# Kernel optimization log

Hardware: AMD Instinct MI355X
Metric: run time of the kernel (lower is better)

Reference implementation:

```python
import jax, jax.numpy as jnp
import numpy as np

N, D, H, E = 50000, 128, 128, 800000


def setup_inputs() -> dict:
    key = jax.random.key(0)
    ks = jax.random.split(key, 12)
    p = lambda k, shape: jax.random.normal(k, shape, dtype=jnp.float32) * 0.02
    z = lambda n: jnp.zeros((n,), jnp.float32)
    return {
        "x1": jax.random.normal(ks[0], (N, D), dtype=jnp.float32),
        "edge_index1": jax.random.randint(ks[1], (2, E), 0, N, dtype=jnp.int32),
        "x2": jax.random.normal(ks[2], (N, D), dtype=jnp.float32),
        "edge_index2": jax.random.randint(ks[3], (2, E), 0, N, dtype=jnp.int32),
        "enc_w1": p(ks[4], (D, H)), "enc_b1": z(H),
        "enc_w2": p(ks[5], (H, H)), "enc_b2": z(H),
        "conv1_w": p(ks[6], (H, H)), "conv1_b": z(H),
        "conv2_w": p(ks[7], (H, H)), "conv2_b": z(H),
        "sim_w1": p(ks[8], (4 * H, H)), "sim_b1": z(H),
        "sim_w2": p(ks[9], (H, 1)), "sim_b2": z(1),
    }


def reference(x1, edge_index1, x2, edge_index2,
              enc_w1, enc_b1, enc_w2, enc_b2,
              conv1_w, conv1_b, conv2_w, conv2_b,
              sim_w1, sim_b1, sim_w2, sim_b2):
    def gcn(x, ei, W, b):
        row, col = ei[0], ei[1]            # [E], [E]
        h = x @ W + b                      # [N, H]
        n = x.shape[0]
        deg = jax.ops.segment_sum(jnp.ones(row.shape[0], h.dtype), row, num_segments=n)
        dis = jnp.where(deg > 0, deg ** -0.5, 0.0)   # deg^-0.5, inf -> 0
        norm = dis[row] * dis[col]         # [E]
        msg = h[col] * norm[:, None]       # gather + per-edge scale, [E, H]
        return jax.ops.segment_sum(msg, row, num_segments=n)  # scatter-add

    def embed(x, ei):
        h = jax.nn.relu(x @ enc_w1 + enc_b1) @ enc_w2 + enc_b2  # encoder MLP
        h = jax.nn.relu(gcn(h, ei, conv1_w, conv1_b))
        h = jax.nn.relu(gcn(h, ei, conv2_w, conv2_b))
        return h.mean(axis=0)              # mean pooling -> [H]

    g1 = embed(x1, edge_index1)
    g2 = embed(x2, edge_index2)
    c = jnp.concatenate([g1, g2, jnp.abs(g1 - g2), g1 * g2], axis=-1)  # [4H]
    return jax.nn.relu(c @ sim_w1 + sim_b1) @ sim_w2 + sim_b2          # [1]
```

## Files before the change

### kernel.cpp

```cpp
#include <hip/hip_runtime.h>

#define HD 128
#define FP8_SCALE 8192.0f
#define FP8_INV   (1.0f / 8192.0f)

typedef _Float16 f16x8 __attribute__((ext_vector_type(8)));
typedef float f32x4 __attribute__((ext_vector_type(4)));
typedef float f32x2 __attribute__((ext_vector_type(2)));

static __device__ __forceinline__ unsigned char f32_to_fp8(float v) {
  return (unsigned char)(__builtin_amdgcn_cvt_pk_fp8_f32(v, v, 0, false) & 0xff);
}

__device__ __forceinline__ void role_map(int bi, int S, int k, int& role, int& rid) {
  int q = bi / k, rem = bi - q * k;
  if (rem == 0 && q < S) { role = 1; rid = q; }
  else { role = 0; int na = q + (rem ? 1 : 0); if (na > S) na = S; rid = bi - na; }
}

__global__ void k_wcvt(const float* __restrict__ w0, const float* __restrict__ w1,
                       const float* __restrict__ w2, const float* __restrict__ w3,
                       _Float16* __restrict__ Wf) {
  int m = blockIdx.x >> 3;
  const float* Wg = (m == 0) ? w0 : (m == 1) ? w1 : (m == 2) ? w2 : w3;
  int idx0 = (blockIdx.x & 7) * 2048 + threadIdx.x * 8;
  float4 u0 = *(const float4*)(Wg + idx0);
  float4 u1 = *(const float4*)(Wg + idx0 + 4);
  int k = idx0 >> 7, n0 = idx0 & 127;
  int kc = k >> 5, q2 = (k >> 3) & 3, j = k & 7;
  _Float16* dst = Wf + (size_t)m * 16384;
  float vv[8] = {u0.x, u0.y, u0.z, u0.w, u1.x, u1.y, u1.z, u1.w};
  #pragma unroll
  for (int d = 0; d < 8; ++d) {
    int n = n0 + d;
    dst[(size_t)(((n >> 4) * 4 + kc) * 64 + 16 * q2 + (n & 15)) * 8 + j] = (_Float16)vv[d];
  }
}

__device__ __forceinline__ void deg_core(int rid, int degB,
    const int* __restrict__ ei0, const int* __restrict__ ei1, int E, int N,
    int* __restrict__ deg2, unsigned short* __restrict__ slot) {
  int g = (rid >= degB);
  int cb = rid - g * degB;
  const int* rows = g ? ei1 : ei0;
  int* deg = deg2 + g * N;
  unsigned short* sl = slot + (size_t)g * E;
  int base = (cb * 256 + threadIdx.x) * 4;
  if (base + 3 < E) {
    int4 r = *(const int4*)(rows + base);
    union { unsigned short us[4]; uint2 v; } s;
    s.us[0] = (unsigned short)atomicAdd(&deg[r.x], 1);
    s.us[1] = (unsigned short)atomicAdd(&deg[r.y], 1);
    s.us[2] = (unsigned short)atomicAdd(&deg[r.z], 1);
    s.us[3] = (unsigned short)atomicAdd(&deg[r.w], 1);
    *(uint2*)(sl + base) = s.v;
  } else {
    for (int e = base; e < E; ++e)
      sl[e] = (unsigned short)atomicAdd(&deg[rows[e]], 1);
  }
}

__device__ __forceinline__ void fill_core(int rid, int fillB,
    const int* __restrict__ ei0, const int* __restrict__ ei1, int E, int N,
    const int* __restrict__ offs, const int* __restrict__ partials,
    const unsigned short* __restrict__ slot, unsigned short* __restrict__ csr_col) {
  int g = (rid >= fillB);
  int cb = rid - g * fillB;
  const int* eg = (g ? ei1 : ei0);
  const int* ob = offs + g * N;
  const unsigned short* sl = slot + (size_t)g * E;
  int gN = g * N;
  int base = (cb * 256 + threadIdx.x) * 4;
  if (base + 3 < E) {
    int4 r = *(const int4*)(eg + base);
    int4 c = *(const int4*)(eg + E + base);
    uint2 sv = *(const uint2*)(sl + base);
    csr_col[ob[r.x] + partials[(gN + r.x) >> 8] + (sv.x & 0xffff)] = (unsigned short)c.x;
    csr_col[ob[r.y] + partials[(gN + r.y) >> 8] + (sv.x >> 16)]    = (unsigned short)c.y;
    csr_col[ob[r.z] + partials[(gN + r.z) >> 8] + (sv.y & 0xffff)] = (unsigned short)c.z;
    csr_col[ob[r.w] + partials[(gN + r.w) >> 8] + (sv.y >> 16)]    = (unsigned short)c.w;
  } else {
    for (int e = base; e < E; ++e)
      csr_col[ob[eg[e]] + partials[(gN + eg[e]) >> 8] + sl[e]] = (unsigned short)eg[E + e];
  }
}

__device__ __forceinline__ void gemm_core(_Float16* lds, int bi,
    const _Float16* __restrict__ Ab, const _Float16* __restrict__ Wf,
    const float* __restrict__ bias, const float* __restrict__ scale,
    unsigned char* __restrict__ Cv, int Ntot) {
  const int tid = threadIdx.x;
  #pragma unroll
  for (int i = 0; i < 8; ++i)
    *(float4*)&lds[tid * 8 + i * 2048] = *(const float4*)&Wf[tid * 8 + i * 2048];
  __syncthreads();

  const int lane = tid & 63, wave = tid >> 6;
  const int n16 = lane & 15, q = lane >> 4;
  const int rowbase = bi * 128 + wave * 32;

  int arow[2];
  #pragma unroll
  for (int t = 0; t < 2; ++t) {
    int r = rowbase + 16 * t + n16;
    arow[t] = (r < Ntot) ? r : (Ntot - 1);
  }
  f32x4 acc[2][8];
  #pragma unroll
  for (int t = 0; t < 2; ++t)
    #pragma unroll
    for (int nt = 0; nt < 8; ++nt) acc[t][nt] = (f32x4){0.f, 0.f, 0.f, 0.f};

  #pragma unroll
  for (int kc = 0; kc < 4; ++kc) {
    f16x8 a[2];
    #pragma unroll
    for (int t = 0; t < 2; ++t)
      a[t] = *(const f16x8*)(Ab + (size_t)arow[t] * HD + kc * 32 + q * 8);
    #pragma unroll
    for (int nt = 0; nt < 8; ++nt) {
      f16x8 b = *(const f16x8*)&lds[(size_t)((nt * 4 + kc) * 64 + lane) * 8];
      #pragma unroll
      for (int t = 0; t < 2; ++t)
        acc[t][nt] = __builtin_amdgcn_mfma_f32_16x16x32_f16(a[t], b, acc[t][nt], 0, 0, 0);
    }
  }
  float bv[8];
  #pragma unroll
  for (int nt = 0; nt < 8; ++nt) bv[nt] = bias[nt * 16 + n16];
  #pragma unroll
  for (int t = 0; t < 2; ++t) {
    #pragma unroll
    for (int r = 0; r < 4; ++r) {
      int row = rowbase + 16 * t + 4 * q + r;
      if (row < Ntot) {
        float s = scale[row];
        #pragma unroll
        for (int nt = 0; nt < 8; ++nt) {
          float v = (acc[t][nt][r] + bv[nt]) * s;
          Cv[(size_t)row * HD + nt * 16 + n16] = f32_to_fp8(v * FP8_SCALE);
        }
      }
    }
  }
}

__device__ __forceinline__ void chain_core(_Float16* act, int bi,
    const float* __restrict__ x0, const float* __restrict__ x1,
    const _Float16* __restrict__ Wf0, const _Float16* __restrict__ Wf1,
    const float* __restrict__ b1, const float* __restrict__ b2,
    _Float16* __restrict__ H, int N, int Ntot) {
  const int tid = threadIdx.x;
  const int lane = tid & 63, wave = tid >> 6;
  const int n16 = lane & 15, q = lane >> 4;
  const int rowbase = bi * 128 + wave * 32;
  _Float16* wact = act + wave * 4352;

  int arow[2];
  #pragma unroll
  for (int t = 0; t < 2; ++t) {
    int r = rowbase + 16 * t + n16;
    arow[t] = (r < Ntot) ? r : (Ntot - 1);
  }
  f32x4 acc[2][8];
  #pragma unroll
  for (int t = 0; t < 2; ++t)
    #pragma unroll
    for (int nt = 0; nt < 8; ++nt) acc[t][nt] = (f32x4){0.f, 0.f, 0.f, 0.f};

  #pragma unroll
  for (int kc = 0; kc < 4; ++kc) {
    f16x8 a[2];
    #pragma unroll
    for (int t = 0; t < 2; ++t) {
      int r = arow[t];
      const float* src = (r < N) ? (x0 + (size_t)r * HD) : (x1 + (size_t)(r - N) * HD);
      float4 u0 = *(const float4*)(src + kc * 32 + q * 8);
      float4 u1 = *(const float4*)(src + kc * 32 + q * 8 + 4);
      union { _Float16 h[8]; f16x8 v; } tmp;
      tmp.h[0] = (_Float16)u0.x; tmp.h[1] = (_Float16)u0.y;
      tmp.h[2] = (_Float16)u0.z; tmp.h[3] = (_Float16)u0.w;
      tmp.h[4] = (_Float16)u1.x; tmp.h[5] = (_Float16)u1.y;
      tmp.h[6] = (_Float16)u1.z; tmp.h[7] = (_Float16)u1.w;
      a[t] = tmp.v;
    }
    #pragma unroll
    for (int nt = 0; nt < 8; ++nt) {
      f16x8 b = *(const f16x8*)&Wf0[(size_t)((nt * 4 + kc) * 64 + lane) * 8];
      #pragma unroll
      for (int t = 0; t < 2; ++t)
        acc[t][nt] = __builtin_amdgcn_mfma_f32_16x16x32_f16(a[t], b, acc[t][nt], 0, 0, 0);
    }
  }
  {
    float bv[8];
    #pragma unroll
    for (int nt = 0; nt < 8; ++nt) bv[nt] = b1[nt * 16 + n16];
    #pragma unroll
    for (int t = 0; t < 2; ++t)
      #pragma unroll
      for (int r = 0; r < 4; ++r)
        #pragma unroll
        for (int nt = 0; nt < 8; ++nt)
          wact[(16 * t + 4 * q + r) * 136 + nt * 16 + n16] =
              (_Float16)fmaxf(acc[t][nt][r] + bv[nt], 0.f);
  }

  #pragma unroll
  for (int t = 0; t < 2; ++t)
    #pragma unroll
    for (int nt = 0; nt < 8; ++nt) acc[t][nt] = (f32x4){0.f, 0.f, 0.f, 0.f};
  #pragma unroll
  for (int kc = 0; kc < 4; ++kc) {
    f16x8 a[2];
    #pragma unroll
    for (int t = 0; t < 2; ++t)
      a[t] = *(const f16x8*)&wact[(16 * t + n16) * 136 + kc * 32 + q * 8];
    #pragma unroll
    for (int nt = 0; nt < 8; ++nt) {
      f16x8 b = *(const f16x8*)&Wf1[(size_t)((nt * 4 + kc) * 64 + lane) * 8];
      #pragma unroll
      for (int t = 0; t < 2; ++t)
        acc[t][nt] = __builtin_amdgcn_mfma_f32_16x16x32_f16(a[t], b, acc[t][nt], 0, 0, 0);
    }
  }
  {
    float bv[8];
    #pragma unroll
    for (int nt = 0; nt < 8; ++nt) bv[nt] = b2[nt * 16 + n16];
    #pragma unroll
    for (int t = 0; t < 2; ++t)
      #pragma unroll
      for (int r = 0; r < 4; ++r) {
        int row = rowbase + 16 * t + 4 * q + r;
        if (row < Ntot)
          #pragma unroll
          for (int nt = 0; nt < 8; ++nt)
            H[(size_t)row * HD + nt * 16 + n16] = (_Float16)(acc[t][nt][r] + bv[nt]);
      }
  }
}

template<bool POOL>
__device__ __forceinline__ void agg_core(float* red, int rid,
    const unsigned char* __restrict__ T8, const int* __restrict__ offs,
    const int* __restrict__ partials, const unsigned short* __restrict__ csr_col,
    const float* __restrict__ dis, _Float16* __restrict__ out,
    float* __restrict__ poolrep, int N, int Ntot, int Etot) {
  const int lane = threadIdx.x & 63;
  const int wave = threadIdx.x >> 6;
  const int gw = rid * 4 + wave;
  const int sub = lane >> 4, c16 = lane & 15;

  float ax[8];
  #pragma unroll
  for (int j = 0; j < 8; ++j) ax[j] = 0.f;

  const int beg = offs[gw] + partials[gw >> 8];
  const int end = (gw + 1 == Ntot) ? Etot : (offs[gw + 1] + partials[(gw + 1) >> 8]);
  const uint2* Tg = (const uint2*)(T8 + (size_t)(gw >= N ? N : 0) * HD);
  for (int e = beg; e < end; e += 16) {
    uint2 v[4];
    #pragma unroll
    for (int gp = 0; gp < 4; ++gp) {
      v[gp] = make_uint2(0, 0);
      if (e + 4 * gp < end) {
        int eg = e + 4 * gp + sub;
        bool valid = (eg < end);
        int ce = valid ? eg : (end - 1);
        int col = csr_col[ce];
        uint2 tv = Tg[(size_t)col * 16 + c16];
        if (valid) v[gp] = tv;
      }
    }
    #pragma unroll
    for (int gp = 0; gp < 4; ++gp) {
      f32x2 p0 = __builtin_amdgcn_cvt_pk_f32_fp8((int)v[gp].x, false);
      f32x2 p1 = __builtin_amdgcn_cvt_pk_f32_fp8((int)v[gp].x, true);
      f32x2 p2 = __builtin_amdgcn_cvt_pk_f32_fp8((int)v[gp].y, false);
      f32x2 p3 = __builtin_amdgcn_cvt_pk_f32_fp8((int)v[gp].y, true);
      ax[0] += p0.x; ax[1] += p0.y;
      ax[2] += p1.x; ax[3] += p1.y;
      ax[4] += p2.x; ax[5] += p2.y;
      ax[6] += p3.x; ax[7] += p3.y;
    }
  }

  #pragma unroll
  for (int j = 0; j < 8; ++j) {
    ax[j] += __shfl_xor(ax[j], 32, 64);
    ax[j] += __shfl_xor(ax[j], 16, 64);
  }
  float dr = dis[gw] * FP8_INV;
  #pragma unroll
  for (int j = 0; j < 8; ++j) ax[j] = fmaxf(ax[j] * dr, 0.f);

  if (!POOL) {
    if (sub == 0) {
      union { uint4 u; _Float16 h[8]; } o;
      #pragma unroll
      for (int j = 0; j < 8; ++j) o.h[j] = (_Float16)ax[j];
      ((uint4*)out)[(size_t)gw * 16 + c16] = o.u;
    }
  } else {
    if (sub == 0) {
      *(float4*)&red[wave * 128 + c16 * 8]     = make_float4(ax[0], ax[1], ax[2], ax[3]);
      *(float4*)&red[wave * 128 + c16 * 8 + 4] = make_float4(ax[4], ax[5], ax[6], ax[7]);
    }
    __syncthreads();
    int t = threadIdx.x;
    if (t < 128) {
      float s = red[t] + red[128 + t] + red[256 + t] + red[384 + t];
      int g = (rid * 4 >= N) ? 1 : 0;
      atomicAdd(&poolrep[(size_t)((rid & 15) * 2 + g) * 128 + t], s);
    }
  }
}

__global__ __launch_bounds__(256, 4) void k_d1(
    const float* __restrict__ x0, const float* __restrict__ x1,
    const _Float16* __restrict__ Wf, const float* __restrict__ b1,
    const float* __restrict__ b2, _Float16* __restrict__ H,
    const int* __restrict__ ei0, const int* __restrict__ ei1, int E, int N, int Ntot,
    int* __restrict__ deg2, unsigned short* __restrict__ slot, int G, int A, int degB) {
  __shared__ _Float16 act[4 * 4352];
  int role, rid;
  role_map(blockIdx.x, G, (A + G) / G, role, rid);
  if (role == 1)
    chain_core(act, rid, x0, x1, Wf, Wf + 16384, b1, b2, H, N, Ntot);
  else
    deg_core(rid, degB, ei0, ei1, E, N, deg2, slot);
}

__global__ __launch_bounds__(256, 2) void k_scan(
    const int* __restrict__ deg2, int* __restrict__ offs, int* __restrict__ partials,
    float* __restrict__ dis, int Ntot, int scanB, int* __restrict__ ctr) {
  __shared__ int s[512];
  __shared__ int lastFlag;
  int rid = blockIdx.x, t = threadIdx.x;
  int i = rid * 256 + t;
  int v = (i < Ntot) ? deg2[i] : 0;
  s[t] = v;
  __syncthreads();
  #pragma unroll
  for (int off = 1; off < 256; off <<= 1) {
    int x = (t >= off) ? s[t - off] : 0;
    __syncthreads();
    s[t] += x;
    __syncthreads();
  }
  if (i < Ntot) {
    offs[i] = s[t] - v;
    dis[i] = (v > 0) ? (1.0f / sqrtf((float)v)) : 0.0f;
  }
  if (t == 255) partials[rid] = s[255];
  __syncthreads();
  if (t == 0) {
    __threadfence();
    lastFlag = (atomicAdd(ctr, 1) == scanB - 1);
  }
  __syncthreads();
  if (lastFlag) {
    __threadfence();
    volatile int* vp = partials;
    int P = scanB;
    int v0 = (t < P) ? vp[t] : 0;
    int v1 = (t + 256 < P) ? vp[t + 256] : 0;
    __syncthreads();
    s[t] = v0;
    s[t + 256] = v1;
    __syncthreads();
    #pragma unroll
    for (int off = 1; off < 256; off <<= 1) {
      int x0 = (t >= off) ? s[t - off] : 0;
      int x1 = (t >= off) ? s[256 + t - off] : 0;
      __syncthreads();
      s[t] += x0;
      s[256 + t] += x1;
      __syncthreads();
    }
    int tot0 = s[255];
    if (t < P) partials[t] = s[t] - v0;
    if (t + 256 < P) partials[t + 256] = s[256 + t] + tot0 - v1;
  }
}

__global__ __launch_bounds__(256, 4) void k_conv1_fill(
    const _Float16* __restrict__ Ain, const _Float16* __restrict__ Wf,
    const float* __restrict__ bias, const float* __restrict__ dis,
    unsigned char* __restrict__ Cout, int Ntot, int G,
    const int* __restrict__ ei0, const int* __restrict__ ei1, int E, int N,
    const int* __restrict__ offs, const int* __restrict__ partials,
    const unsigned short* __restrict__ slot, unsigned short* __restrict__ csr_col,
    int fillB) {
  __shared__ _Float16 lds[16384];
  int role, rid;
  role_map(blockIdx.x, G, 3, role, rid);
  if (role == 1)
    gemm_core(lds, rid, Ain, Wf, bias, dis, Cout, Ntot);
  else
    fill_core(rid, fillB, ei0, ei1, E, N, offs, partials, slot, csr_col);
}

__global__ __launch_bounds__(256) void k_agg(
    const unsigned char* __restrict__ T8, const int* __restrict__ offs,
    const int* __restrict__ partials, const unsigned short* __restrict__ csr_col,
    const float* __restrict__ dis, _Float16* __restrict__ out, int N, int Ntot, int Etot) {
  agg_core<false>(nullptr, blockIdx.x, T8, offs, partials, csr_col, dis,
                  out, nullptr, N, Ntot, Etot);
}

__global__ __launch_bounds__(256, 4) void k_gemm(
    const _Float16* __restrict__ Ain, const _Float16* __restrict__ Wf,
    const float* __restrict__ bias, const float* __restrict__ dis,
    unsigned char* __restrict__ Cout, int Ntot) {
  __shared__ _Float16 lds[16384];
  gemm_core(lds, blockIdx.x, Ain, Wf, bias, dis, Cout, Ntot);
}

__global__ __launch_bounds__(256) void k_agg_pool(
    const unsigned char* __restrict__ T8, const int* __restrict__ offs,
    const int* __restrict__ partials, const unsigned short* __restrict__ csr_col,
    const float* __restrict__ dis, float* __restrict__ poolrep,
    int N, int Ntot, int Etot) {
  __shared__ float red[512];
  agg_core<true>(red, blockIdx.x, T8, offs, partials, csr_col, dis,
                 nullptr, poolrep, N, Ntot, Etot);
}

__global__ void k_final(const float* __restrict__ poolrep,
                        const float* __restrict__ W1, const float* __restrict__ b1,
                        const float* __restrict__ W2, const float* __restrict__ b2,
                        float* __restrict__ out, float invN) {
  __shared__ float cs[512];
  __shared__ float red[2];
  int t = threadIdx.x;
  float g1 = 0.f, g2 = 0.f;
  #pragma unroll
  for (int r = 0; r < 16; ++r) {
    g1 += poolrep[r * 256 + t];
    g2 += poolrep[r * 256 + 128 + t];
  }
  g1 *= invN;
  g2 *= invN;
  cs[t] = g1;
  cs[128 + t] = g2;
  cs[256 + t] = fabsf(g1 - g2);
  cs[384 + t] = g1 * g2;
  __syncthreads();
  float acc = b1[t];
  #pragma unroll 8
  for (int i = 0; i < 512; ++i) acc = fmaf(cs[i], W1[(size_t)i * HD + t], acc);
  float h = fmaxf(acc, 0.f);
  float v = h * W2[t];
  #pragma unroll
  for (int off = 32; off > 0; off >>= 1) v += __shfl_down(v, off, 64);
  if ((t & 63) == 0) red[t >> 6] = v;
  __syncthreads();
  if (t == 0) out[0] = red[0] + red[1] + b2[0];
}

extern "C" void kernel_launch(void* const* d_in, const int* in_sizes, int n_in,
                              void* d_out, int out_size, void* d_ws, size_t ws_size,
                              hipStream_t stream) {
  const float* x1     = (const float*)d_in[0];
  const int*   ei1    = (const int*)d_in[1];
  const float* x2     = (const float*)d_in[2];
  const int*   ei2    = (const int*)d_in[3];
  const float* W_in[4] = {(const float*)d_in[4], (const float*)d_in[6],
                          (const float*)d_in[8], (const float*)d_in[10]};
  const float* B_in[4] = {(const float*)d_in[5], (const float*)d_in[7],
                          (const float*)d_in[9], (const float*)d_in[11]};
  const float* sim_w1 = (const float*)d_in[12];
  const float* sim_b1 = (const float*)d_in[13];
  const float* sim_w2 = (const float*)d_in[14];
  const float* sim_b2 = (const float*)d_in[15];

  const int N = in_sizes[0] / HD;
  const int E = in_sizes[1] / 2;
  const int Ntot = 2 * N;

  _Float16* sp = (_Float16*)d_ws;
  _Float16* bufA = sp; sp += (size_t)Ntot * HD;
  _Float16* bufC = sp; sp += (size_t)Ntot * HD;
  unsigned char* bufT8 = (unsigned char*)sp;
  sp += (size_t)Ntot * HD / 2;
  _Float16* WfB  = sp; sp += 4 * 16384;
  float* fp = (float*)sp;
  float* dis     = fp; fp += Ntot;
  float* poolrep = fp; fp += 16 * 256;
  int* ip = (int*)fp;
  int* ctrs     = ip; ip += 8;
  int* deg2     = ip; ip += Ntot;
  int* offs     = ip; ip += Ntot;
  int* partials = ip; ip += 512;
  ip = (int*)(((uintptr_t)ip + 15) & ~(uintptr_t)15);
  unsigned short* slot = (unsigned short*)ip;
  unsigned short* csr_col = slot + 2 * (size_t)E;

  const int G1    = (Ntot + 127) / 128;
  const int scanB = (Ntot + 255) / 256;
  const int aggB  = Ntot / 4;
  const int degB  = ((E + 3) / 4 + 255) / 256;
  const int fillB = degB;

  hipMemsetAsync(poolrep, 0, (16 * 256 + 8 + Ntot) * sizeof(float), stream);

  k_wcvt<<<32, 256, 0, stream>>>(W_in[0], W_in[1], W_in[2], W_in[3], WfB);

  k_d1<<<2 * degB + G1, 256, 0, stream>>>(
      x1, x2, WfB, B_in[0], B_in[1], bufA, ei1, ei2, E, N, Ntot,
      deg2, slot, G1, 2 * degB, degB);

  k_scan<<<scanB, 256, 0, stream>>>(deg2, offs, partials, dis, Ntot, scanB, ctrs);

  k_conv1_fill<<<2 * fillB + G1, 256, 0, stream>>>(
      bufA, WfB + 2 * 16384, B_in[2], dis, bufT8, Ntot, G1,
      ei1, ei2, E, N, offs, partials, slot, csr_col, fillB);

  k_agg<<<aggB, 256, 0, stream>>>(bufT8, offs, partials, csr_col, dis, bufC, N, Ntot, 2 * E);

  k_gemm<<<G1, 256, 0, stream>>>(bufC, WfB + 3 * 16384, B_in[3], dis, bufT8, Ntot);

  k_agg_pool<<<aggB, 256, 0, stream>>>(bufT8, offs, partials, csr_col, dis, poolrep,
                                       N, Ntot, 2 * E);

  k_final<<<1, 128, 0, stream>>>(poolrep, sim_w1, sim_b1, sim_w2, sim_b2,
                                 (float*)d_out, 1.0f / (float)N);
}
```

Before: 387.5 us.

## Split degree counting into own kernel, fuse scan with encoder chain; widen aggregation unroll

Degree counting becomes a standalone kernel, and the prefix scan is merged with the encoder MLP chain into a single launch via role mapping. This hides the scan behind the GEMM work instead of running it as a separate serial kernel. The aggregation loop also now processes 32 edges per iteration instead of 16, putting more gathers in flight. The cost is higher register use in the aggregation kernel. The scan blocks now reuse the chain's shared memory buffer, and the chain now runs after degree counting rather than overlapping with it.

```diff
diff --git a/kernel.cpp b/kernel.cpp
--- a/kernel.cpp
+++ b/kernel.cpp
@@ -37,9 +37,10 @@
   }
 }
 
-__device__ __forceinline__ void deg_core(int rid, int degB,
+__global__ __launch_bounds__(256) void k_deg(
     const int* __restrict__ ei0, const int* __restrict__ ei1, int E, int N,
-    int* __restrict__ deg2, unsigned short* __restrict__ slot) {
+    int* __restrict__ deg2, unsigned short* __restrict__ slot, int degB) {
+  int rid = blockIdx.x;
   int g = (rid >= degB);
   int cb = rid - g * degB;
   const int* rows = g ? ei1 : ei0;
@@ -241,103 +242,22 @@
   }
 }
 
-template<bool POOL>
-__device__ __forceinline__ void agg_core(float* red, int rid,
-    const unsigned char* __restrict__ T8, const int* __restrict__ offs,
-    const int* __restrict__ partials, const unsigned short* __restrict__ csr_col,
-    const float* __restrict__ dis, _Float16* __restrict__ out,
-    float* __restrict__ poolrep, int N, int Ntot, int Etot) {
-  const int lane = threadIdx.x & 63;
-  const int wave = threadIdx.x >> 6;
-  const int gw = rid * 4 + wave;
-  const int sub = lane >> 4, c16 = lane & 15;
-
-  float ax[8];
-  #pragma unroll
-  for (int j = 0; j < 8; ++j) ax[j] = 0.f;
-
-  const int beg = offs[gw] + partials[gw >> 8];
-  const int end = (gw + 1 == Ntot) ? Etot : (offs[gw + 1] + partials[(gw + 1) >> 8]);
-  const uint2* Tg = (const uint2*)(T8 + (size_t)(gw >= N ? N : 0) * HD);
-  for (int e = beg; e < end; e += 16) {
-    uint2 v[4];
-    #pragma unroll
-    for (int gp = 0; gp < 4; ++gp) {
-      v[gp] = make_uint2(0, 0);
-      if (e + 4 * gp < end) {
-        int eg = e + 4 * gp + sub;
-        bool valid = (eg < end);
-        int ce = valid ? eg : (end - 1);
-        int col = csr_col[ce];
-        uint2 tv = Tg[(size_t)col * 16 + c16];
-        if (valid) v[gp] = tv;
-      }
-    }
-    #pragma unroll
-    for (int gp = 0; gp < 4; ++gp) {
-      f32x2 p0 = __builtin_amdgcn_cvt_pk_f32_fp8((int)v[gp].x, false);
-      f32x2 p1 = __builtin_amdgcn_cvt_pk_f32_fp8((int)v[gp].x, true);
-      f32x2 p2 = __builtin_amdgcn_cvt_pk_f32_fp8((int)v[gp].y, false);
-      f32x2 p3 = __builtin_amdgcn_cvt_pk_f32_fp8((int)v[gp].y, true);
-      ax[0] += p0.x; ax[1] += p0.y;
-      ax[2] += p1.x; ax[3] += p1.y;
-      ax[4] += p2.x; ax[5] += p2.y;
-      ax[6] += p3.x; ax[7] += p3.y;
-    }
-  }
-
-  #pragma unroll
-  for (int j = 0; j < 8; ++j) {
-    ax[j] += __shfl_xor(ax[j], 32, 64);
-    ax[j] += __shfl_xor(ax[j], 16, 64);
-  }
-  float dr = dis[gw] * FP8_INV;
-  #pragma unroll
-  for (int j = 0; j < 8; ++j) ax[j] = fmaxf(ax[j] * dr, 0.f);
-
-  if (!POOL) {
-    if (sub == 0) {
-      union { uint4 u; _Float16 h[8]; } o;
-      #pragma unroll
-      for (int j = 0; j < 8; ++j) o.h[j] = (_Float16)ax[j];
-      ((uint4*)out)[(size_t)gw * 16 + c16] = o.u;
-    }
-  } else {
-    if (sub == 0) {
-      *(float4*)&red[wave * 128 + c16 * 8]     = make_float4(ax[0], ax[1], ax[2], ax[3]);
-      *(float4*)&red[wave * 128 + c16 * 8 + 4] = make_float4(ax[4], ax[5], ax[6], ax[7]);
-    }
-    __syncthreads();
-    int t = threadIdx.x;
-    if (t < 128) {
-      float s = red[t] + red[128 + t] + red[256 + t] + red[384 + t];
-      int g = (rid * 4 >= N) ? 1 : 0;
-      atomicAdd(&poolrep[(size_t)((rid & 15) * 2 + g) * 128 + t], s);
-    }
-  }
-}
-
-__global__ __launch_bounds__(256, 4) void k_d1(
+__global__ __launch_bounds__(256, 4) void k_chain_scan(
     const float* __restrict__ x0, const float* __restrict__ x1,
     const _Float16* __restrict__ Wf, const float* __restrict__ b1,
-    const float* __restrict__ b2, _Float16* __restrict__ H,
-    const int* __restrict__ ei0, const int* __restrict__ ei1, int E, int N, int Ntot,
-    int* __restrict__ deg2, unsigned short* __restrict__ slot, int G, int A, int degB) {
+    const float* __restrict__ b2, _Float16* __restrict__ H, int N, int Ntot, int G,
+    const int* __restrict__ deg2, int* __restrict__ offs, int* __restrict__ partials,
+    float* __restrict__ dis, int scanB, int* __restrict__ ctr) {
   __shared__ _Float16 act[4 * 4352];
+  __shared__ int lastFlag;
   int role, rid;
-  role_map(blockIdx.x, G, (A + G) / G, role, rid);
-  if (role == 1)
+  role_map(blockIdx.x, scanB, (scanB + G) / scanB, role, rid);
+  if (role == 0) {
     chain_core(act, rid, x0, x1, Wf, Wf + 16384, b1, b2, H, N, Ntot);
-  else
-    deg_core(rid, degB, ei0, ei1, E, N, deg2, slot);
-}
-
-__global__ __launch_bounds__(256, 2) void k_scan(
-    const int* __restrict__ deg2, int* __restrict__ offs, int* __restrict__ partials,
-    float* __restrict__ dis, int Ntot, int scanB, int* __restrict__ ctr) {
-  __shared__ int s[512];
-  __shared__ int lastFlag;
-  int rid = blockIdx.x, t = threadIdx.x;
+    return;
+  }
+  int* s = (int*)act;
+  int t = threadIdx.x;
   int i = rid * 256 + t;
   int v = (i < Ntot) ? deg2[i] : 0;
   s[t] = v;
@@ -382,6 +302,82 @@
     int tot0 = s[255];
     if (t < P) partials[t] = s[t] - v0;
     if (t + 256 < P) partials[t + 256] = s[256 + t] + tot0 - v1;
+  }
+}
+
+template<bool POOL>
+__device__ __forceinline__ void agg_core(float* red, int rid,
+    const unsigned char* __restrict__ T8, const int* __restrict__ offs,
+    const int* __restrict__ partials, const unsigned short* __restrict__ csr_col,
+    const float* __restrict__ dis, _Float16* __restrict__ out,
+    float* __restrict__ poolrep, int N, int Ntot, int Etot) {
+  const int lane = threadIdx.x & 63;
+  const int wave = threadIdx.x >> 6;
+  const int gw = rid * 4 + wave;
+  const int sub = lane >> 4, c16 = lane & 15;
+
+  float ax[8];
+  #pragma unroll
+  for (int j = 0; j < 8; ++j) ax[j] = 0.f;
+
+  const int beg = offs[gw] + partials[gw >> 8];
+  const int end = (gw + 1 == Ntot) ? Etot : (offs[gw + 1] + partials[(gw + 1) >> 8]);
+  const uint2* Tg = (const uint2*)(T8 + (size_t)(gw >= N ? N : 0) * HD);
+  for (int e = beg; e < end; e += 32) {
+    uint2 v[8];
+    #pragma unroll
+    for (int gp = 0; gp < 8; ++gp) {
+      v[gp] = make_uint2(0, 0);
+      if (e + 4 * gp < end) {
+        int eg = e + 4 * gp + sub;
+        bool valid = (eg < end);
+        int ce = valid ? eg : (end - 1);
+        int col = csr_col[ce];
+        uint2 tv = Tg[(size_t)col * 16 + c16];
+        if (valid) v[gp] = tv;
+      }
+    }
+    #pragma unroll
+    for (int gp = 0; gp < 8; ++gp) {
+      f32x2 p0 = __builtin_amdgcn_cvt_pk_f32_fp8((int)v[gp].x, false);
+      f32x2 p1 = __builtin_amdgcn_cvt_pk_f32_fp8((int)v[gp].x, true);
+      f32x2 p2 = __builtin_amdgcn_cvt_pk_f32_fp8((int)v[gp].y, false);
+      f32x2 p3 = __builtin_amdgcn_cvt_pk_f32_fp8((int)v[gp].y, true);
+      ax[0] += p0.x; ax[1] += p0.y;
+      ax[2] += p1.x; ax[3] += p1.y;
+      ax[4] += p2.x; ax[5] += p2.y;
+      ax[6] += p3.x; ax[7] += p3.y;
+    }
+  }
+
+  #pragma unroll
+  for (int j = 0; j < 8; ++j) {
+    ax[j] += __shfl_xor(ax[j], 32, 64);
+    ax[j] += __shfl_xor(ax[j], 16, 64);
+  }
+  float dr = dis[gw] * FP8_INV;
+  #pragma unroll
+  for (int j = 0; j < 8; ++j) ax[j] = fmaxf(ax[j] * dr, 0.f);
+
+  if (!POOL) {
+    if (sub == 0) {
+      union { uint4 u; _Float16 h[8]; } o;
+      #pragma unroll
+      for (int j = 0; j < 8; ++j) o.h[j] = (_Float16)ax[j];
+      ((uint4*)out)[(size_t)gw * 16 + c16] = o.u;
+    }
+  } else {
+    if (sub == 0) {
+      *(float4*)&red[wave * 128 + c16 * 8]     = make_float4(ax[0], ax[1], ax[2], ax[3]);
+      *(float4*)&red[wave * 128 + c16 * 8 + 4] = make_float4(ax[4], ax[5], ax[6], ax[7]);
+    }
+    __syncthreads();
+    int t = threadIdx.x;
+    if (t < 128) {
+      float s = red[t] + red[128 + t] + red[256 + t] + red[384 + t];
+      int g = (rid * 4 >= N) ? 1 : 0;
+      atomicAdd(&poolrep[(size_t)((rid & 15) * 2 + g) * 128 + t], s);
+    }
   }
 }
 
@@ -508,11 +504,11 @@
 
   k_wcvt<<<32, 256, 0, stream>>>(W_in[0], W_in[1], W_in[2], W_in[3], WfB);
 
-  k_d1<<<2 * degB + G1, 256, 0, stream>>>(
-      x1, x2, WfB, B_in[0], B_in[1], bufA, ei1, ei2, E, N, Ntot,
-      deg2, slot, G1, 2 * degB, degB);
-
-  k_scan<<<scanB, 256, 0, stream>>>(deg2, offs, partials, dis, Ntot, scanB, ctrs);
+  k_deg<<<2 * degB, 256, 0, stream>>>(ei1, ei2, E, N, deg2, slot, degB);
+
+  k_chain_scan<<<scanB + G1, 256, 0, stream>>>(
+      x1, x2, WfB, B_in[0], B_in[1], bufA, N, Ntot, G1,
+      deg2, offs, partials, dis, scanB, ctrs);
 
   k_conv1_fill<<<2 * fillB + G1, 256, 0, stream>>>(
       bufA, WfB + 2 * 16384, B_in[2], dis, bufT8, Ntot, G1,
```

Measured after the change: 394.0 us. No clear change (+1.7%).
